# Optimization experiments

Measured on AMD Instinct MI355X. Metric: run time of the kernel, lower is better.

Reference implementation:

```python
import jax, jax.numpy as jnp
import numpy as np

WS = 7          # window size
DIM = 192
HEADS = 6
NW = 64         # number of windows per image (mask leading dim)
NC = 3          # n_contrast (q and kv)
B_ = 1024       # num_windows * batch


def _relative_position_index(ws):
    coords = np.stack(np.meshgrid(np.arange(ws), np.arange(ws), indexing='ij'))  # (2, ws, ws)
    cf = coords.reshape(2, -1)                       # (2, ws*ws)
    rel = cf[:, :, None] - cf[:, None, :]            # (2, N, N)
    rel = rel.transpose(1, 2, 0).copy()              # (N, N, 2)
    rel[:, :, 0] += ws - 1
    rel[:, :, 1] += ws - 1
    rel[:, :, 0] *= 2 * ws - 1
    return rel.sum(-1)                               # (N, N) int

REL_IDX = jnp.asarray(_relative_position_index(WS))


def setup_inputs() -> dict:
    key = jax.random.key(0)
    ks = jax.random.split(key, 13)
    f32 = jnp.float32
    inp = {
        'x_q': jax.random.normal(ks[0], (B_, NC, WS, WS, DIM), f32),
        'x_k': jax.random.normal(ks[1], (B_, NC, WS, WS, DIM), f32),
        'x_v': jax.random.normal(ks[2], (B_, NC, WS, WS, DIM), f32),
        'mask': jax.random.normal(ks[3], (NW, WS * WS, WS * WS), f32),
        # Linear weights stored torch-style: (out_features, in_features)
        'q_w': jax.random.normal(ks[4], (DIM, DIM), f32) * 0.02,
        'q_b': jnp.zeros((DIM,), f32),
        'k_w': jax.random.normal(ks[5], (DIM, DIM), f32) * 0.02,
        'k_b': jnp.zeros((DIM,), f32),
        'v_w': jax.random.normal(ks[6], (DIM, DIM), f32) * 0.02,
        'v_b': jnp.zeros((DIM,), f32),
        'proj_w': jax.random.normal(ks[7], (DIM, DIM), f32) * 0.02,
        'proj_b': jnp.zeros((DIM,), f32),
        'bias_table': jax.random.normal(ks[8], ((2 * WS - 1) ** 2, HEADS), f32) * 0.02,
    }
    return inp


def reference(x_q, x_k, x_v, mask, q_w, q_b, k_w, k_b, v_w, v_b, proj_w, proj_b, bias_table):
    Bw, ncq, Wh, Ww, C = x_q.shape
    nckv = x_k.shape[1]
    H = HEADS
    hd = C // H
    Nq = ncq * Wh * Ww
    Nkv = nckv * Wh * Ww

    xq = x_q.reshape(Bw, Nq, C)
    xk = x_k.reshape(Bw, Nkv, C)
    xv = x_v.reshape(Bw, Nkv, C)

    q = (xq @ q_w.T + q_b).reshape(Bw, Nq, H, hd).transpose(0, 2, 1, 3)   # (B_, H, Nq, hd)
    k = (xk @ k_w.T + k_b).reshape(Bw, Nkv, H, hd).transpose(0, 2, 1, 3)
    v = (xv @ v_w.T + v_b).reshape(Bw, Nkv, H, hd).transpose(0, 2, 1, 3)

    scale = hd ** (-0.5)
    attn = jnp.einsum('bhqd,bhkd->bhqk', q * scale, k)                    # (B_, H, Nq, Nkv)

    Nwin = Wh * Ww
    bias = bias_table[REL_IDX.reshape(-1)].reshape(Nwin, Nwin, H)
    bias = bias.transpose(2, 0, 1)                                        # (H, Nwin, Nwin)
    bias = jnp.tile(bias, (1, ncq, nckv))                                 # (H, Nq, Nkv)
    attn = attn + bias[None]

    nW = mask.shape[0]
    m = jnp.tile(mask, (1, ncq, nckv))                                    # (nW, Nq, Nkv)
    attn = attn.reshape(Bw // nW, nW, H, Nq, Nkv) + m[None, :, None]
    attn = attn.reshape(Bw, H, Nq, Nkv)
    attn = jax.nn.softmax(attn, axis=-1)

    out = jnp.einsum('bhqk,bhkd->bhqd', attn, v)                          # (B_, H, Nq, hd)
    out = out.transpose(0, 2, 1, 3).reshape(Bw, Nq, C)
    out = out @ proj_w.T + proj_b
    return out.reshape(Bw, ncq, Wh, Ww, C)
```

## Files before the change

kernel.cpp:

```cpp
#include <hip/hip_runtime.h>
#include <stdint.h>

#define ROWS 150528
#define QSCALE 0.17677669529663687f
#define L2E 1.44269504088896f

typedef __attribute__((ext_vector_type(8))) __bf16 bf16x8;
typedef __attribute__((ext_vector_type(4))) __bf16 bf16x4;
typedef __attribute__((ext_vector_type(4))) float f32x4;
typedef __attribute__((ext_vector_type(4))) float f4;

static __device__ __forceinline__ f32x4 mfma_bf16(bf16x8 a, bf16x8 b, f32x4 c) {
  return __builtin_amdgcn_mfma_f32_16x16x32_bf16(a, b, c, 0, 0, 0);
}

static __device__ __forceinline__ uint32_t pack_bf16(float a, float b) {
  uint16_t ux = __builtin_bit_cast(uint16_t, (__bf16)a);
  uint16_t uy = __builtin_bit_cast(uint16_t, (__bf16)b);
  return (uint32_t)ux | ((uint32_t)uy << 16);
}

__global__ void cvt4(const float* s0, const float* s1, const float* s2, const float* s3,
                     __bf16* d0, __bf16* d1, __bf16* d2, __bf16* d3) {
  const int y = blockIdx.y;
  const float* s = y == 0 ? s0 : y == 1 ? s1 : y == 2 ? s2 : s3;
  __bf16* d = y == 0 ? d0 : y == 1 ? d1 : y == 2 ? d2 : d3;
  int i = blockIdx.x * 256 + threadIdx.x;
  f4 v = ((const f4*)s)[i];
  bf16x4 b;
  b[0] = (__bf16)v[0]; b[1] = (__bf16)v[1]; b[2] = (__bf16)v[2]; b[3] = (__bf16)v[3];
  ((bf16x4*)d)[i] = b;
}

__global__ void bmpre(const float* __restrict__ maskp, const float* __restrict__ btab,
                      float* __restrict__ bmall) {
  const int win = blockIdx.x, h = blockIdx.y;
  float* dst = bmall + ((size_t)(win * 6 + h)) * 2800;
  for (int i = threadIdx.x; i < 2796; i += 256) {
    int q = i / 57, ke = i - q * 57;
    int k = ke >= 49 ? ke - 49 : ke;
    if (q > 48) q = 48;
    int qi = q / 7, qj = q - qi * 7, ki = k / 7, kj = k - ki * 7;
    int rel = (qi - ki + 6) * 13 + (qj - kj + 6);
    dst[i] = (maskp[win * 2401 + q * 49 + k] + btab[rel * 6 + h]) * L2E;
  }
}

template<bool IN_F32, bool OUT_F32>
static __device__ __forceinline__
void gemm3t(const void* __restrict__ Xv, const __bf16* __restrict__ Wb,
            const float* __restrict__ bias, void* __restrict__ Ov, float scale,
            __bf16* Xs )
{
  const int tid = threadIdx.x;
  const int wv = tid >> 6, lane = tid & 63, lr = lane & 15, lg = lane >> 4;

  bf16x8 wf[3][6];
  float bcol[3];
  #pragma unroll
  for (int t = 0; t < 3; ++t) {
    const int nt = wv + 4 * t;
    const __bf16* wr = &Wb[(nt * 16 + lr) * 192 + lg * 8];
    #pragma unroll
    for (int kk = 0; kk < 6; ++kk) wf[t][kk] = *(const bf16x8*)&wr[kk * 32];
    bcol[t] = bias[nt * 16 + lr] * scale;
  }

  const size_t ti0 = (size_t)blockIdx.x * 3;

  if (IN_F32) {
    const f4* X4 = (const f4*)Xv + ti0 * 64 * 48;
    #pragma unroll
    for (int p = 0; p < 12; ++p) {
      int i = tid + p * 256;
      int r = i / 48, c = i % 48;
      f4 v = X4[i];
      bf16x4 bb;
      bb[0] = (__bf16)v[0]; bb[1] = (__bf16)v[1]; bb[2] = (__bf16)v[2]; bb[3] = (__bf16)v[3];
      *(bf16x4*)&Xs[r * 200 + c * 4] = bb;
    }
  } else {
    const __bf16* X = (const __bf16*)Xv;
    #pragma unroll
    for (int p = 0; p < 6; ++p) {
      int i = tid + p * 256;
      int r = i / 24, c8 = i % 24;
      int hh = c8 >> 2, sub = c8 & 3;
      *(bf16x8*)&Xs[r * 200 + c8 * 8] =
          *(const bf16x8*)&X[((size_t)hh * ROWS + ti0 * 64 + r) * 32 + sub * 8];
    }
  }
  __syncthreads();

  #pragma unroll
  for (int it = 0; it < 3; ++it) {
    const size_t row0 = (ti0 + it) * 64;

    f4 pf[12];
    bf16x8 pf8[6];
    if (it < 2) {
      if (IN_F32) {
        const f4* X4n = (const f4*)Xv + (row0 + 64) * 48;
        #pragma unroll
        for (int p = 0; p < 12; ++p) pf[p] = X4n[tid + p * 256];
      } else {
        const __bf16* X = (const __bf16*)Xv;
        #pragma unroll
        for (int p = 0; p < 6; ++p) {
          int i = tid + p * 256;
          int r = i / 24, c8 = i % 24;
          int hh = c8 >> 2, sub = c8 & 3;
          pf8[p] = *(const bf16x8*)&X[((size_t)hh * ROWS + row0 + 64 + r) * 32 + sub * 8];
        }
      }
    }

    #pragma unroll
    for (int rg = 0; rg < 4; ++rg) {
      bf16x8 a[6];
      const __bf16* xr = &Xs[(rg * 16 + lr) * 200 + lg * 8];
      #pragma unroll
      for (int kk = 0; kk < 6; ++kk) a[kk] = *(const bf16x8*)&xr[kk * 32];
      const size_t grow = row0 + rg * 16 + lg * 4;
      #pragma unroll
      for (int t = 0; t < 3; ++t) {
        f32x4 acc = {0.f, 0.f, 0.f, 0.f};
        #pragma unroll
        for (int kk = 0; kk < 6; ++kk) acc = mfma_bf16(a[kk], wf[t][kk], acc);
        const int nt = wv + 4 * t;
        if (OUT_F32) {
          const int col = nt * 16 + lr;
          #pragma unroll
          for (int j = 0; j < 4; ++j)
            ((float*)Ov)[(grow + j) * 192 + col] = acc[j] * scale + bcol[t];
        } else {
          const int hh = nt >> 1, c32 = (nt & 1) * 16 + lr;
          #pragma unroll
          for (int j = 0; j < 4; ++j)
            ((__bf16*)Ov)[((size_t)hh * ROWS + grow + j) * 32 + c32] =
                (__bf16)(acc[j] * scale + bcol[t]);
        }
      }
    }

    if (it < 2) {
      __syncthreads();
      if (IN_F32) {
        #pragma unroll
        for (int p = 0; p < 12; ++p) {
          int i = tid + p * 256;
          int r = i / 48, c = i % 48;
          bf16x4 bb;
          bb[0] = (__bf16)pf[p][0]; bb[1] = (__bf16)pf[p][1];
          bb[2] = (__bf16)pf[p][2]; bb[3] = (__bf16)pf[p][3];
          *(bf16x4*)&Xs[r * 200 + c * 4] = bb;
        }
      } else {
        #pragma unroll
        for (int p = 0; p < 6; ++p) {
          int i = tid + p * 256;
          int r = i / 24, c8 = i % 24;
          *(bf16x8*)&Xs[r * 200 + c8 * 8] = pf8[p];
        }
      }
      __syncthreads();
    }
  }
}

__global__ __launch_bounds__(256, 2)
void qkvgemm(const float* __restrict__ xq, const float* __restrict__ xk,
             const float* __restrict__ xv,
             const __bf16* __restrict__ wq, const __bf16* __restrict__ wk,
             const __bf16* __restrict__ wv,
             const float* __restrict__ bq, const float* __restrict__ bk,
             const float* __restrict__ bv,
             __bf16* __restrict__ oq, __bf16* __restrict__ ok,
             __bf16* __restrict__ ov)
{
  __shared__ __align__(16) __bf16 Xs[64 * 200];
  const int y = blockIdx.y;
  const float* x = y == 0 ? xq : y == 1 ? xk : xv;
  const __bf16* w = y == 0 ? wq : y == 1 ? wk : wv;
  const float* bi = y == 0 ? bq : y == 1 ? bk : bv;
  __bf16* o = y == 0 ? oq : y == 1 ? ok : ov;
  const float scale = y == 0 ? (QSCALE * L2E) : 1.f;
  gemm3t<true, false>(x, w, bi, o, scale, Xs);
}

__global__ __launch_bounds__(256, 2)
void projgemm(const __bf16* __restrict__ X, const __bf16* __restrict__ Wb,
              const float* __restrict__ bias, float* __restrict__ Ov)
{
  __shared__ __align__(16) __bf16 Xs[64 * 200];
  gemm3t<false, true>(X, Wb, bias, Ov, 1.f, Xs);
}

__global__ __launch_bounds__(320, 5)
void attn8(const __bf16* __restrict__ Q, const __bf16* __restrict__ K,
           const __bf16* __restrict__ V, __bf16* __restrict__ O,
           const float* __restrict__ bmall)
{
  __shared__ __align__(16) __bf16 Ks[160 * 40];
  __shared__ __align__(16) __bf16 Vt[32 * 168];
  __shared__ __align__(16) float bm2[2796];

  const int b = blockIdx.x, h = blockIdx.y;
  const int tid = threadIdx.x;
  const size_t hb = (size_t)h * ROWS + (size_t)b * 147;
  const int wv = tid >> 6, lane = tid & 63;
  const int lr = lane & 15, lg = lane >> 4;

  bf16x8 qf = *(const bf16x8*)&Q[(hb + wv * 16 + lr) * 32 + lg * 8];

  {
    const f4* bsrc = (const f4*)(bmall + (size_t)((b & 63) * 6 + h) * 2800);
    for (int i = tid; i < 699; i += 320) ((f4*)bm2)[i] = bsrc[i];
  }
  for (int i = tid; i < 588; i += 320) {
    int k = i >> 2, c = i & 3;
    int phys = (k & ~31) | (((k >> 2) & 1) << 4) | (((k >> 3) & 3) << 2) | (k & 3);
    *(bf16x8*)&Ks[phys * 40 + c * 8] = *(const bf16x8*)&K[(hb + k) * 32 + c * 8];
  }
  for (int t = tid; t < 588; t += 320) {
    int key = t >> 2, dblk = t & 3;
    bf16x8 v = *(const bf16x8*)&V[(hb + key) * 32 + dblk * 8];
    #pragma unroll
    for (int e = 0; e < 8; ++e) Vt[(dblk * 8 + e) * 168 + key] = v[e];
  }
  for (int i = tid; i < 32 * 13; i += 320) {
    int d = i / 13, key = 147 + (i - (i / 13) * 13);
    Vt[d * 168 + key] = (__bf16)0.f;
  }
  __syncthreads();

  #pragma unroll
  for (int t = 0; t < 2; ++t) {
    const int mt = wv + 5 * t;

    bf16x8 qn = qf;
    if (t == 0) {
      int qr = (wv + 5) * 16 + lr; if (qr > 146) qr = 146;
      qn = *(const bf16x8*)&Q[(hb + qr) * 32 + lg * 8];
    }

    int r = mt * 16 + lr;
    int q49 = r; if (q49 >= 98) q49 -= 98; if (q49 >= 49) q49 -= 49;
    const float* bmrow = &bm2[q49 * 57];

    f32x4 o0 = {0.f,0.f,0.f,0.f}, o1 = {0.f,0.f,0.f,0.f};
    float sum = 0.f;
    int kb = lg * 8;
    #pragma unroll
    for (int s = 0; s < 5; ++s) {
      const f32x4 z = {0.f,0.f,0.f,0.f};
      f32x4 st0 = mfma_bf16(*(const bf16x8*)&Ks[(s * 32 + lr) * 40 + lg * 8], qf, z);
      f32x4 st1 = mfma_bf16(*(const bf16x8*)&Ks[(s * 32 + 16 + lr) * 40 + lg * 8], qf, z);
      const float* bp = bmrow + kb;
      #pragma unroll
      for (int j = 0; j < 4; ++j) { st0[j] += bp[j]; st1[j] += bp[4 + j]; }
      if (s == 4) {
        #pragma unroll
        for (int j = 0; j < 4; ++j) {
          if (lg * 8 + j >= 19) st0[j] = -1e30f;
          if (lg * 8 + j >= 15) st1[j] = -1e30f;
        }
      }
      #pragma unroll
      for (int j = 0; j < 4; ++j) { st0[j] = exp2f(st0[j]); sum += st0[j]; }
      #pragma unroll
      for (int j = 0; j < 4; ++j) { st1[j] = exp2f(st1[j]); sum += st1[j]; }
      union { bf16x8 v; uint32_t w[4]; } pu;
      pu.w[0] = pack_bf16(st0[0], st0[1]);
      pu.w[1] = pack_bf16(st0[2], st0[3]);
      pu.w[2] = pack_bf16(st1[0], st1[1]);
      pu.w[3] = pack_bf16(st1[2], st1[3]);
      bf16x8 v0 = *(const bf16x8*)&Vt[lr * 168 + s * 32 + lg * 8];
      bf16x8 v1 = *(const bf16x8*)&Vt[(16 + lr) * 168 + s * 32 + lg * 8];
      o0 = mfma_bf16(pu.v, v0, o0);
      o1 = mfma_bf16(pu.v, v1, o1);
      kb += 32; if (kb >= 49) kb -= 49;
    }
    sum += __shfl_xor(sum, 16);
    sum += __shfl_xor(sum, 32);
    const float rinv = 1.f / sum;
    #pragma unroll
    for (int j = 0; j < 4; ++j) {
      const int qa = mt * 16 + lg * 4 + j;
      const float rj = __shfl(rinv, lg * 4 + j);
      if (qa < 147) {
        const size_t base = (hb + qa) * 32;
        O[base + lr]      = (__bf16)(o0[j] * rj);
        O[base + 16 + lr] = (__bf16)(o1[j] * rj);
      }
    }
    qf = qn;
  }
}

extern "C" void kernel_launch(void* const* d_in, const int* in_sizes, int n_in,
                              void* d_out, int out_size, void* d_ws, size_t ws_size,
                              hipStream_t stream) {
  (void)in_sizes; (void)n_in; (void)out_size;
  const float* x_q  = (const float*)d_in[0];
  const float* x_k  = (const float*)d_in[1];
  const float* x_v  = (const float*)d_in[2];
  const float* maskp= (const float*)d_in[3];
  const float* q_w  = (const float*)d_in[4];
  const float* q_b  = (const float*)d_in[5];
  const float* k_w  = (const float*)d_in[6];
  const float* k_b  = (const float*)d_in[7];
  const float* v_w  = (const float*)d_in[8];
  const float* v_b  = (const float*)d_in[9];
  const float* p_w  = (const float*)d_in[10];
  const float* p_b  = (const float*)d_in[11];
  const float* btab = (const float*)d_in[12];

  char* ws = (char*)d_ws;
  float* bmall = (float*)ws;
  const size_t bmsz = (size_t)64 * 6 * 2800 * sizeof(float);
  char* wsp = ws + bmsz;
  const size_t wsz = 36864 * sizeof(__bf16);
  __bf16* wq  = (__bf16*)wsp;
  __bf16* wk  = (__bf16*)(wsp + wsz);
  __bf16* wvp = (__bf16*)(wsp + 2 * wsz);
  __bf16* wp  = (__bf16*)(wsp + 3 * wsz);
  char* bufs = wsp + 4 * wsz;
  const size_t sz = (size_t)ROWS * 192 * sizeof(__bf16);
  __bf16* qb = (__bf16*)bufs;
  __bf16* kb = (__bf16*)(bufs + sz);
  __bf16* vb = (__bf16*)(bufs + 2 * sz);
  const size_t need4 = bmsz + 4 * wsz + 4 * sz;
  __bf16* ob = (ws_size >= need4) ? (__bf16*)(bufs + 3 * sz) : qb;

  cvt4<<<dim3(36, 4), 256, 0, stream>>>(q_w, k_w, v_w, p_w, wq, wk, wvp, wp);
  bmpre<<<dim3(64, 6), 256, 0, stream>>>(maskp, btab, bmall);

  qkvgemm<<<dim3(ROWS / 192, 3), 256, 0, stream>>>(x_q, x_k, x_v, wq, wk, wvp,
                                                   q_b, k_b, v_b, qb, kb, vb);

  attn8<<<dim3(1024, 6), 320, 0, stream>>>(qb, kb, vb, ob, bmall);

  projgemm<<<ROWS / 192, 256, 0, stream>>>(ob, wp, p_b, (float*)d_out);
}
```

Baseline: 264.0 us.

## Fuse QKV projection into per-window attention kernel, keeping K/V in LDS

Replaces the separate QKV GEMM and attention kernels with one kernel per window. It projects K and V into shared memory and Q into registers, then runs all six heads' attention from there. The Q weight rows are permuted and pre-scaled so the projected Q lands directly in MFMA operand layout. This removes the bf16 Q/K/V round-trip through global memory and one launch. In exchange each block uses a lot of LDS (about 140 KB) and 640 threads, which limits occupancy, and every block reloads the weight matrices.

```diff
diff --git a/kernel.cpp b/kernel.cpp
--- a/kernel.cpp
+++ b/kernel.cpp
@@ -4,11 +4,13 @@
 #define ROWS 150528
 #define QSCALE 0.17677669529663687f
 #define L2E 1.44269504088896f
+#define QS (QSCALE * L2E)
 
 typedef __attribute__((ext_vector_type(8))) __bf16 bf16x8;
 typedef __attribute__((ext_vector_type(4))) __bf16 bf16x4;
 typedef __attribute__((ext_vector_type(4))) float f32x4;
 typedef __attribute__((ext_vector_type(4))) float f4;
+typedef __attribute__((ext_vector_type(2))) uint32_t u32x2;
 
 static __device__ __forceinline__ f32x4 mfma_bf16(bf16x8 a, bf16x8 b, f32x4 c) {
   return __builtin_amdgcn_mfma_f32_16x16x32_bf16(a, b, c, 0, 0, 0);
@@ -20,16 +22,36 @@
   return (uint32_t)ux | ((uint32_t)uy << 16);
 }
 
+static __device__ __forceinline__ int sigma(int p) {
+  int ct = p >> 4, m = p & 15;
+  return (ct >> 1) * 32 + ((m >> 2) << 3) + ((ct & 1) << 2) + (m & 3);
+}
+
 __global__ void cvt4(const float* s0, const float* s1, const float* s2, const float* s3,
                      __bf16* d0, __bf16* d1, __bf16* d2, __bf16* d3) {
   const int y = blockIdx.y;
-  const float* s = y == 0 ? s0 : y == 1 ? s1 : y == 2 ? s2 : s3;
-  __bf16* d = y == 0 ? d0 : y == 1 ? d1 : y == 2 ? d2 : d3;
   int i = blockIdx.x * 256 + threadIdx.x;
+  if (y == 0) {
+    int p = i / 48, c = i - p * 48;
+    f4 v = ((const f4*)s0)[sigma(p) * 48 + c];
+    bf16x4 b;
+    #pragma unroll
+    for (int e = 0; e < 4; ++e) b[e] = (__bf16)(v[e] * QS);
+    ((bf16x4*)d0)[i] = b;
+    return;
+  }
+  const float* s = y == 1 ? s1 : y == 2 ? s2 : s3;
+  __bf16* d = y == 1 ? d1 : y == 2 ? d2 : d3;
   f4 v = ((const f4*)s)[i];
   bf16x4 b;
-  b[0] = (__bf16)v[0]; b[1] = (__bf16)v[1]; b[2] = (__bf16)v[2]; b[3] = (__bf16)v[3];
+  #pragma unroll
+  for (int e = 0; e < 4; ++e) b[e] = (__bf16)v[e];
   ((bf16x4*)d)[i] = b;
+}
+
+__global__ void bprep(const float* __restrict__ qb, float* __restrict__ bqp) {
+  int p = threadIdx.x;
+  if (p < 192) bqp[p] = qb[sigma(p)] * QS;
 }
 
 __global__ void bmpre(const float* __restrict__ maskp, const float* __restrict__ btab,
@@ -46,11 +68,170 @@
   }
 }
 
+__global__ __launch_bounds__(640, 3)
+void fqkattn(const float* __restrict__ xq, const float* __restrict__ xk,
+             const float* __restrict__ xv,
+             const __bf16* __restrict__ wqp, const __bf16* __restrict__ wkb,
+             const __bf16* __restrict__ wvb,
+             const float* __restrict__ bqp, const float* __restrict__ bk,
+             const float* __restrict__ bv,
+             __bf16* __restrict__ O, const float* __restrict__ bmall)
+{
+  __shared__ __align__(16) __bf16 Ks[38400];
+  __shared__ __align__(16) __bf16 Vt[32256];
+
+  const int b = blockIdx.x;
+  const int tid = threadIdx.x;
+  const int wvn = tid >> 6;
+  const int lane = tid & 63, lr = lane & 15, lg = lane >> 4;
+  const size_t bw = (size_t)b * 147;
+  const int row = wvn * 16 + lr;
+  const int rowc = row > 146 ? 146 : row;
+  const int phys = (row & ~31) | (((row >> 2) & 1) << 4) | (((row >> 3) & 3) << 2) | (row & 3);
+
+  bf16x8 a[6];
+  auto loadA = [&](const float* base) {
+    f4 p0[12];
+    #pragma unroll
+    for (int kk = 0; kk < 6; ++kk) {
+      p0[2 * kk]     = *(const f4*)(base + kk * 32);
+      p0[2 * kk + 1] = *(const f4*)(base + kk * 32 + 4);
+    }
+    #pragma unroll
+    for (int kk = 0; kk < 6; ++kk)
+      #pragma unroll
+      for (int e = 0; e < 4; ++e) {
+        a[kk][e]     = (__bf16)p0[2 * kk][e];
+        a[kk][4 + e] = (__bf16)p0[2 * kk + 1][e];
+      }
+  };
+
+  loadA(&xk[(bw + rowc) * 192 + lg * 8]);
+  for (int ct = 0; ct < 12; ++ct) {
+    bf16x8 wf[6];
+    const __bf16* wr = &wkb[(ct * 16 + lr) * 192 + lg * 8];
+    #pragma unroll
+    for (int kk = 0; kk < 6; ++kk) wf[kk] = *(const bf16x8*)&wr[kk * 32];
+    f32x4 acc = {0.f, 0.f, 0.f, 0.f};
+    #pragma unroll
+    for (int kk = 0; kk < 6; ++kk) acc = mfma_bf16(wf[kk], a[kk], acc);
+    f4 bb = *(const f4*)&bk[ct * 16 + 4 * lg];
+    u32x2 pw;
+    pw[0] = pack_bf16(acc[0] + bb[0], acc[1] + bb[1]);
+    pw[1] = pack_bf16(acc[2] + bb[2], acc[3] + bb[3]);
+    *(u32x2*)&Ks[(ct >> 1) * 6400 + phys * 40 + (ct & 1) * 16 + 4 * lg] = pw;
+  }
+
+  loadA(&xv[(bw + rowc) * 192 + lg * 8]);
+  for (int ct = 0; ct < 12; ++ct) {
+    bf16x8 wf[6];
+    const __bf16* wr = &wvb[(ct * 16 + lr) * 192 + lg * 8];
+    #pragma unroll
+    for (int kk = 0; kk < 6; ++kk) wf[kk] = *(const bf16x8*)&wr[kk * 32];
+    f32x4 acc = {0.f, 0.f, 0.f, 0.f};
+    #pragma unroll
+    for (int kk = 0; kk < 6; ++kk) acc = mfma_bf16(wf[kk], a[kk], acc);
+    f4 bb = *(const f4*)&bv[ct * 16 + 4 * lg];
+    const int d0 = (ct & 1) * 16 + 4 * lg;
+    __bf16* vb8 = &Vt[(ct >> 1) * 5376 + row];
+    #pragma unroll
+    for (int j = 0; j < 4; ++j) vb8[(d0 + j) * 168] = (__bf16)(acc[j] + bb[j]);
+  }
+
+  loadA(&xq[(bw + rowc) * 192 + lg * 8]);
+  bf16x8 qf6[6];
+  #pragma unroll
+  for (int hh = 0; hh < 6; ++hh) {
+    union { bf16x8 v; uint32_t w[4]; } q;
+    #pragma unroll
+    for (int half = 0; half < 2; ++half) {
+      const int ct = hh * 2 + half;
+      bf16x8 wf[6];
+      const __bf16* wr = &wqp[(ct * 16 + lr) * 192 + lg * 8];
+      #pragma unroll
+      for (int kk = 0; kk < 6; ++kk) wf[kk] = *(const bf16x8*)&wr[kk * 32];
+      f32x4 acc = {0.f, 0.f, 0.f, 0.f};
+      #pragma unroll
+      for (int kk = 0; kk < 6; ++kk) acc = mfma_bf16(wf[kk], a[kk], acc);
+      f4 bb = *(const f4*)&bqp[ct * 16 + 4 * lg];
+      q.w[half * 2]     = pack_bf16(acc[0] + bb[0], acc[1] + bb[1]);
+      q.w[half * 2 + 1] = pack_bf16(acc[2] + bb[2], acc[3] + bb[3]);
+    }
+    qf6[hh] = q.v;
+  }
+  __syncthreads();
+
+  int q49 = row; if (q49 >= 98) q49 -= 98; if (q49 >= 49) q49 -= 49;
+  int off[5];
+  {
+    int kb = lg * 8;
+    #pragma unroll
+    for (int s = 0; s < 5; ++s) { off[s] = q49 * 57 + kb; kb += 32; if (kb >= 49) kb -= 49; }
+  }
+  const float* bmb = bmall + (size_t)((b & 63) * 6) * 2800;
+
+  #pragma unroll
+  for (int h = 0; h < 6; ++h) {
+    const float* bmh = bmb + h * 2800;
+    f4 bb0[5], bb1[5];
+    #pragma unroll
+    for (int s = 0; s < 5; ++s) {
+      bb0[s] = *(const f4*)(bmh + off[s]);
+      bb1[s] = *(const f4*)(bmh + off[s] + 4);
+    }
+    const __bf16* kbase = &Ks[h * 6400];
+    const __bf16* vbase = &Vt[h * 5376];
+    f32x4 o0 = {0.f,0.f,0.f,0.f}, o1 = {0.f,0.f,0.f,0.f};
+    float sum = 0.f;
+    #pragma unroll
+    for (int s = 0; s < 5; ++s) {
+      const f32x4 z = {0.f,0.f,0.f,0.f};
+      f32x4 st0 = mfma_bf16(*(const bf16x8*)&kbase[(s * 32 + lr) * 40 + lg * 8], qf6[h], z);
+      f32x4 st1 = mfma_bf16(*(const bf16x8*)&kbase[(s * 32 + 16 + lr) * 40 + lg * 8], qf6[h], z);
+      #pragma unroll
+      for (int j = 0; j < 4; ++j) { st0[j] += bb0[s][j]; st1[j] += bb1[s][j]; }
+      if (s == 4) {
+        #pragma unroll
+        for (int j = 0; j < 4; ++j) {
+          if (lg * 8 + j >= 19) st0[j] = -1e30f;
+          if (lg * 8 + j >= 15) st1[j] = -1e30f;
+        }
+      }
+      #pragma unroll
+      for (int j = 0; j < 4; ++j) { st0[j] = exp2f(st0[j]); sum += st0[j]; }
+      #pragma unroll
+      for (int j = 0; j < 4; ++j) { st1[j] = exp2f(st1[j]); sum += st1[j]; }
+      union { bf16x8 v; uint32_t w[4]; } pu;
+      pu.w[0] = pack_bf16(st0[0], st0[1]);
+      pu.w[1] = pack_bf16(st0[2], st0[3]);
+      pu.w[2] = pack_bf16(st1[0], st1[1]);
+      pu.w[3] = pack_bf16(st1[2], st1[3]);
+      bf16x8 v0 = *(const bf16x8*)&vbase[lr * 168 + s * 32 + lg * 8];
+      bf16x8 v1 = *(const bf16x8*)&vbase[(16 + lr) * 168 + s * 32 + lg * 8];
+      o0 = mfma_bf16(pu.v, v0, o0);
+      o1 = mfma_bf16(pu.v, v1, o1);
+    }
+    sum += __shfl_xor(sum, 16);
+    sum += __shfl_xor(sum, 32);
+    const float rinv = 1.f / sum;
+    #pragma unroll
+    for (int j = 0; j < 4; ++j) {
+      const int qa = wvn * 16 + lg * 4 + j;
+      const float rj = __shfl(rinv, lg * 4 + j);
+      if (qa < 147) {
+        const size_t base = ((size_t)h * ROWS + bw + qa) * 32;
+        O[base + lr]      = (__bf16)(o0[j] * rj);
+        O[base + 16 + lr] = (__bf16)(o1[j] * rj);
+      }
+    }
+  }
+}
+
 template<bool IN_F32, bool OUT_F32>
 static __device__ __forceinline__
 void gemm3t(const void* __restrict__ Xv, const __bf16* __restrict__ Wb,
             const float* __restrict__ bias, void* __restrict__ Ov, float scale,
-            __bf16* Xs )
+            __bf16* Xs)
 {
   const int tid = threadIdx.x;
   const int wv = tid >> 6, lane = tid & 63, lr = lane & 15, lg = lane >> 4;
@@ -68,18 +249,7 @@
 
   const size_t ti0 = (size_t)blockIdx.x * 3;
 
-  if (IN_F32) {
-    const f4* X4 = (const f4*)Xv + ti0 * 64 * 48;
-    #pragma unroll
-    for (int p = 0; p < 12; ++p) {
-      int i = tid + p * 256;
-      int r = i / 48, c = i % 48;
-      f4 v = X4[i];
-      bf16x4 bb;
-      bb[0] = (__bf16)v[0]; bb[1] = (__bf16)v[1]; bb[2] = (__bf16)v[2]; bb[3] = (__bf16)v[3];
-      *(bf16x4*)&Xs[r * 200 + c * 4] = bb;
-    }
-  } else {
+  {
     const __bf16* X = (const __bf16*)Xv;
     #pragma unroll
     for (int p = 0; p < 6; ++p) {
@@ -96,22 +266,15 @@
   for (int it = 0; it < 3; ++it) {
     const size_t row0 = (ti0 + it) * 64;
 
-    f4 pf[12];
     bf16x8 pf8[6];
     if (it < 2) {
-      if (IN_F32) {
-        const f4* X4n = (const f4*)Xv + (row0 + 64) * 48;
-        #pragma unroll
-        for (int p = 0; p < 12; ++p) pf[p] = X4n[tid + p * 256];
-      } else {
-        const __bf16* X = (const __bf16*)Xv;
-        #pragma unroll
-        for (int p = 0; p < 6; ++p) {
-          int i = tid + p * 256;
-          int r = i / 24, c8 = i % 24;
-          int hh = c8 >> 2, sub = c8 & 3;
-          pf8[p] = *(const bf16x8*)&X[((size_t)hh * ROWS + row0 + 64 + r) * 32 + sub * 8];
-        }
+      const __bf16* X = (const __bf16*)Xv;
+      #pragma unroll
+      for (int p = 0; p < 6; ++p) {
+        int i = tid + p * 256;
+        int r = i / 24, c8 = i % 24;
+        int hh = c8 >> 2, sub = c8 & 3;
+        pf8[p] = *(const bf16x8*)&X[((size_t)hh * ROWS + row0 + 64 + r) * 32 + sub * 8];
       }
     }
 
@@ -128,64 +291,24 @@
         #pragma unroll
         for (int kk = 0; kk < 6; ++kk) acc = mfma_bf16(a[kk], wf[t][kk], acc);
         const int nt = wv + 4 * t;
-        if (OUT_F32) {
-          const int col = nt * 16 + lr;
-          #pragma unroll
-          for (int j = 0; j < 4; ++j)
-            ((float*)Ov)[(grow + j) * 192 + col] = acc[j] * scale + bcol[t];
-        } else {
-          const int hh = nt >> 1, c32 = (nt & 1) * 16 + lr;
-          #pragma unroll
-          for (int j = 0; j < 4; ++j)
-            ((__bf16*)Ov)[((size_t)hh * ROWS + grow + j) * 32 + c32] =
-                (__bf16)(acc[j] * scale + bcol[t]);
-        }
+        const int col = nt * 16 + lr;
+        #pragma unroll
+        for (int j = 0; j < 4; ++j)
+          ((float*)Ov)[(grow + j) * 192 + col] = acc[j] * scale + bcol[t];
       }
     }
 
     if (it < 2) {
       __syncthreads();
-      if (IN_F32) {
-        #pragma unroll
-        for (int p = 0; p < 12; ++p) {
-          int i = tid + p * 256;
-          int r = i / 48, c = i % 48;
-          bf16x4 bb;
-          bb[0] = (__bf16)pf[p][0]; bb[1] = (__bf16)pf[p][1];
-          bb[2] = (__bf16)pf[p][2]; bb[3] = (__bf16)pf[p][3];
-          *(bf16x4*)&Xs[r * 200 + c * 4] = bb;
-        }
-      } else {
-        #pragma unroll
-        for (int p = 0; p < 6; ++p) {
-          int i = tid + p * 256;
-          int r = i / 24, c8 = i % 24;
-          *(bf16x8*)&Xs[r * 200 + c8 * 8] = pf8[p];
-        }
+      #pragma unroll
+      for (int p = 0; p < 6; ++p) {
+        int i = tid + p * 256;
+        int r = i / 24, c8 = i % 24;
+        *(bf16x8*)&Xs[r * 200 + c8 * 8] = pf8[p];
       }
       __syncthreads();
     }
   }
-}
-
-__global__ __launch_bounds__(256, 2)
-void qkvgemm(const float* __restrict__ xq, const float* __restrict__ xk,
-             const float* __restrict__ xv,
-             const __bf16* __restrict__ wq, const __bf16* __restrict__ wk,
-             const __bf16* __restrict__ wv,
-             const float* __restrict__ bq, const float* __restrict__ bk,
-             const float* __restrict__ bv,
-             __bf16* __restrict__ oq, __bf16* __restrict__ ok,
-             __bf16* __restrict__ ov)
-{
-  __shared__ __align__(16) __bf16 Xs[64 * 200];
-  const int y = blockIdx.y;
-  const float* x = y == 0 ? xq : y == 1 ? xk : xv;
-  const __bf16* w = y == 0 ? wq : y == 1 ? wk : wv;
-  const float* bi = y == 0 ? bq : y == 1 ? bk : bv;
-  __bf16* o = y == 0 ? oq : y == 1 ? ok : ov;
-  const float scale = y == 0 ? (QSCALE * L2E) : 1.f;
-  gemm3t<true, false>(x, w, bi, o, scale, Xs);
 }
 
 __global__ __launch_bounds__(256, 2)
@@ -196,112 +319,10 @@
   gemm3t<false, true>(X, Wb, bias, Ov, 1.f, Xs);
 }
 
-__global__ __launch_bounds__(320, 5)
-void attn8(const __bf16* __restrict__ Q, const __bf16* __restrict__ K,
-           const __bf16* __restrict__ V, __bf16* __restrict__ O,
-           const float* __restrict__ bmall)
-{
-  __shared__ __align__(16) __bf16 Ks[160 * 40];
-  __shared__ __align__(16) __bf16 Vt[32 * 168];
-  __shared__ __align__(16) float bm2[2796];
-
-  const int b = blockIdx.x, h = blockIdx.y;
-  const int tid = threadIdx.x;
-  const size_t hb = (size_t)h * ROWS + (size_t)b * 147;
-  const int wv = tid >> 6, lane = tid & 63;
-  const int lr = lane & 15, lg = lane >> 4;
-
-  bf16x8 qf = *(const bf16x8*)&Q[(hb + wv * 16 + lr) * 32 + lg * 8];
-
-  {
-    const f4* bsrc = (const f4*)(bmall + (size_t)((b & 63) * 6 + h) * 2800);
-    for (int i = tid; i < 699; i += 320) ((f4*)bm2)[i] = bsrc[i];
-  }
-  for (int i = tid; i < 588; i += 320) {
-    int k = i >> 2, c = i & 3;
-    int phys = (k & ~31) | (((k >> 2) & 1) << 4) | (((k >> 3) & 3) << 2) | (k & 3);
-    *(bf16x8*)&Ks[phys * 40 + c * 8] = *(const bf16x8*)&K[(hb + k) * 32 + c * 8];
-  }
-  for (int t = tid; t < 588; t += 320) {
-    int key = t >> 2, dblk = t & 3;
-    bf16x8 v = *(const bf16x8*)&V[(hb + key) * 32 + dblk * 8];
-    #pragma unroll
-    for (int e = 0; e < 8; ++e) Vt[(dblk * 8 + e) * 168 + key] = v[e];
-  }
-  for (int i = tid; i < 32 * 13; i += 320) {
-    int d = i / 13, key = 147 + (i - (i / 13) * 13);
-    Vt[d * 168 + key] = (__bf16)0.f;
-  }
-  __syncthreads();
-
-  #pragma unroll
-  for (int t = 0; t < 2; ++t) {
-    const int mt = wv + 5 * t;
-
-    bf16x8 qn = qf;
-    if (t == 0) {
-      int qr = (wv + 5) * 16 + lr; if (qr > 146) qr = 146;
-      qn = *(const bf16x8*)&Q[(hb + qr) * 32 + lg * 8];
-    }
-
-    int r = mt * 16 + lr;
-    int q49 = r; if (q49 >= 98) q49 -= 98; if (q49 >= 49) q49 -= 49;
-    const float* bmrow = &bm2[q49 * 57];
-
-    f32x4 o0 = {0.f,0.f,0.f,0.f}, o1 = {0.f,0.f,0.f,0.f};
-    float sum = 0.f;
-    int kb = lg * 8;
-    #pragma unroll
-    for (int s = 0; s < 5; ++s) {
-      const f32x4 z = {0.f,0.f,0.f,0.f};
-      f32x4 st0 = mfma_bf16(*(const bf16x8*)&Ks[(s * 32 + lr) * 40 + lg * 8], qf, z);
-      f32x4 st1 = mfma_bf16(*(const bf16x8*)&Ks[(s * 32 + 16 + lr) * 40 + lg * 8], qf, z);
-      const float* bp = bmrow + kb;
-      #pragma unroll
-      for (int j = 0; j < 4; ++j) { st0[j] += bp[j]; st1[j] += bp[4 + j]; }
-      if (s == 4) {
-        #pragma unroll
-        for (int j = 0; j < 4; ++j) {
-          if (lg * 8 + j >= 19) st0[j] = -1e30f;
-          if (lg * 8 + j >= 15) st1[j] = -1e30f;
-        }
-      }
-      #pragma unroll
-      for (int j = 0; j < 4; ++j) { st0[j] = exp2f(st0[j]); sum += st0[j]; }
-      #pragma unroll
-      for (int j = 0; j < 4; ++j) { st1[j] = exp2f(st1[j]); sum += st1[j]; }
-      union { bf16x8 v; uint32_t w[4]; } pu;
-      pu.w[0] = pack_bf16(st0[0], st0[1]);
-      pu.w[1] = pack_bf16(st0[2], st0[3]);
-      pu.w[2] = pack_bf16(st1[0], st1[1]);
-      pu.w[3] = pack_bf16(st1[2], st1[3]);
-      bf16x8 v0 = *(const bf16x8*)&Vt[lr * 168 + s * 32 + lg * 8];
-      bf16x8 v1 = *(const bf16x8*)&Vt[(16 + lr) * 168 + s * 32 + lg * 8];
-      o0 = mfma_bf16(pu.v, v0, o0);
-      o1 = mfma_bf16(pu.v, v1, o1);
-      kb += 32; if (kb >= 49) kb -= 49;
-    }
-    sum += __shfl_xor(sum, 16);
-    sum += __shfl_xor(sum, 32);
-    const float rinv = 1.f / sum;
-    #pragma unroll
-    for (int j = 0; j < 4; ++j) {
-      const int qa = mt * 16 + lg * 4 + j;
-      const float rj = __shfl(rinv, lg * 4 + j);
-      if (qa < 147) {
-        const size_t base = (hb + qa) * 32;
-        O[base + lr]      = (__bf16)(o0[j] * rj);
-        O[base + 16 + lr] = (__bf16)(o1[j] * rj);
-      }
-    }
-    qf = qn;
-  }
-}
-
 extern "C" void kernel_launch(void* const* d_in, const int* in_sizes, int n_in,
                               void* d_out, int out_size, void* d_ws, size_t ws_size,
                               hipStream_t stream) {
-  (void)in_sizes; (void)n_in; (void)out_size;
+  (void)in_sizes; (void)n_in; (void)out_size; (void)ws_size;
   const float* x_q  = (const float*)d_in[0];
   const float* x_k  = (const float*)d_in[1];
   const float* x_v  = (const float*)d_in[2];
@@ -321,25 +342,19 @@
   const size_t bmsz = (size_t)64 * 6 * 2800 * sizeof(float);
   char* wsp = ws + bmsz;
   const size_t wsz = 36864 * sizeof(__bf16);
-  __bf16* wq  = (__bf16*)wsp;
-  __bf16* wk  = (__bf16*)(wsp + wsz);
-  __bf16* wvp = (__bf16*)(wsp + 2 * wsz);
-  __bf16* wp  = (__bf16*)(wsp + 3 * wsz);
-  char* bufs = wsp + 4 * wsz;
-  const size_t sz = (size_t)ROWS * 192 * sizeof(__bf16);
-  __bf16* qb = (__bf16*)bufs;
-  __bf16* kb = (__bf16*)(bufs + sz);
-  __bf16* vb = (__bf16*)(bufs + 2 * sz);
-  const size_t need4 = bmsz + 4 * wsz + 4 * sz;
-  __bf16* ob = (ws_size >= need4) ? (__bf16*)(bufs + 3 * sz) : qb;
-
-  cvt4<<<dim3(36, 4), 256, 0, stream>>>(q_w, k_w, v_w, p_w, wq, wk, wvp, wp);
+  __bf16* wqp = (__bf16*)wsp;
+  __bf16* wkb = (__bf16*)(wsp + wsz);
+  __bf16* wvb = (__bf16*)(wsp + 2 * wsz);
+  __bf16* wpb = (__bf16*)(wsp + 3 * wsz);
+  float* bqp  = (float*)(wsp + 4 * wsz);
+  __bf16* ob  = (__bf16*)(wsp + 4 * wsz + 1024);
+
+  cvt4<<<dim3(36, 4), 256, 0, stream>>>(q_w, k_w, v_w, p_w, wqp, wkb, wvb, wpb);
+  bprep<<<1, 192, 0, stream>>>(q_b, bqp);
   bmpre<<<dim3(64, 6), 256, 0, stream>>>(maskp, btab, bmall);
 
-  qkvgemm<<<dim3(ROWS / 192, 3), 256, 0, stream>>>(x_q, x_k, x_v, wq, wk, wvp,
-                                                   q_b, k_b, v_b, qb, kb, vb);
-
-  attn8<<<dim3(1024, 6), 320, 0, stream>>>(qb, kb, vb, ob, bmall);
-
-  projgemm<<<ROWS / 192, 256, 0, stream>>>(ob, wp, p_b, (float*)d_out);
-}
+  fqkattn<<<1024, 640, 0, stream>>>(x_q, x_k, x_v, wqp, wkb, wvb,
+                                    bqp, k_b, v_b, ob, bmall);
+
+  projgemm<<<ROWS / 192, 256, 0, stream>>>(ob, wpb, p_b, (float*)d_out);
+}
```

New measurement: 425.8 us. +61.3%, slower.

## Double-buffer GEMM LDS tiles, double rows per block, merge prep kernels

Applied to the files above, without the earlier changes.

Merges the weight-conversion and bias/mask precompute kernels into one launch to save a launch. The QKV and projection GEMMs now process six 64-row tiles per block instead of three, with a double-buffered shared-memory tile that drops one barrier per iteration. Each block now uses twice the LDS and launch bounds drop to one block per SM-equivalent, so occupancy falls and the grid halves, which may reduce latency hiding and load balance.

```diff
diff --git a/kernel.cpp b/kernel.cpp
--- a/kernel.cpp
+++ b/kernel.cpp
@@ -20,35 +20,40 @@
   return (uint32_t)ux | ((uint32_t)uy << 16);
 }
 
-__global__ void cvt4(const float* s0, const float* s1, const float* s2, const float* s3,
-                     __bf16* d0, __bf16* d1, __bf16* d2, __bf16* d3) {
-  const int y = blockIdx.y;
-  const float* s = y == 0 ? s0 : y == 1 ? s1 : y == 2 ? s2 : s3;
-  __bf16* d = y == 0 ? d0 : y == 1 ? d1 : y == 2 ? d2 : d3;
-  int i = blockIdx.x * 256 + threadIdx.x;
-  f4 v = ((const f4*)s)[i];
-  bf16x4 b;
-  b[0] = (__bf16)v[0]; b[1] = (__bf16)v[1]; b[2] = (__bf16)v[2]; b[3] = (__bf16)v[3];
-  ((bf16x4*)d)[i] = b;
-}
-
-__global__ void bmpre(const float* __restrict__ maskp, const float* __restrict__ btab,
-                      float* __restrict__ bmall) {
-  const int win = blockIdx.x, h = blockIdx.y;
-  float* dst = bmall + ((size_t)(win * 6 + h)) * 2800;
-  for (int i = threadIdx.x; i < 2796; i += 256) {
-    int q = i / 57, ke = i - q * 57;
-    int k = ke >= 49 ? ke - 49 : ke;
-    if (q > 48) q = 48;
-    int qi = q / 7, qj = q - qi * 7, ki = k / 7, kj = k - ki * 7;
-    int rel = (qi - ki + 6) * 13 + (qj - kj + 6);
-    dst[i] = (maskp[win * 2401 + q * 49 + k] + btab[rel * 6 + h]) * L2E;
+__global__ void prep(const float* __restrict__ q_w, const float* __restrict__ k_w,
+                     const float* __restrict__ v_w, const float* __restrict__ p_w,
+                     __bf16* __restrict__ wq, __bf16* __restrict__ wk,
+                     __bf16* __restrict__ wv, __bf16* __restrict__ wp,
+                     const float* __restrict__ maskp, const float* __restrict__ btab,
+                     float* __restrict__ bmall) {
+  const int bid = blockIdx.x;
+  if (bid < 144) {
+    const int y = bid / 36;
+    const float* s = y == 0 ? q_w : y == 1 ? k_w : y == 2 ? v_w : p_w;
+    __bf16* d = y == 0 ? wq : y == 1 ? wk : y == 2 ? wv : wp;
+    int i = (bid % 36) * 256 + threadIdx.x;
+    f4 v = ((const f4*)s)[i];
+    bf16x4 b;
+    b[0] = (__bf16)v[0]; b[1] = (__bf16)v[1]; b[2] = (__bf16)v[2]; b[3] = (__bf16)v[3];
+    ((bf16x4*)d)[i] = b;
+  } else {
+    const int idx = bid - 144;
+    const int win = idx / 6, h = idx - win * 6;
+    float* dst = bmall + ((size_t)idx) * 2800;
+    for (int i = threadIdx.x; i < 2796; i += 256) {
+      int q = i / 57, ke = i - q * 57;
+      int k = ke >= 49 ? ke - 49 : ke;
+      if (q > 48) q = 48;
+      int qi = q / 7, qj = q - qi * 7, ki = k / 7, kj = k - ki * 7;
+      int rel = (qi - ki + 6) * 13 + (qj - kj + 6);
+      dst[i] = (maskp[win * 2401 + q * 49 + k] + btab[rel * 6 + h]) * L2E;
+    }
   }
 }
 
 template<bool IN_F32, bool OUT_F32>
 static __device__ __forceinline__
-void gemm3t(const void* __restrict__ Xv, const __bf16* __restrict__ Wb,
+void gemm6t(const void* __restrict__ Xv, const __bf16* __restrict__ Wb,
             const float* __restrict__ bias, void* __restrict__ Ov, float scale,
             __bf16* Xs )
 {
@@ -66,7 +71,7 @@
     bcol[t] = bias[nt * 16 + lr] * scale;
   }
 
-  const size_t ti0 = (size_t)blockIdx.x * 3;
+  const size_t ti0 = (size_t)blockIdx.x * 6;
 
   if (IN_F32) {
     const f4* X4 = (const f4*)Xv + ti0 * 64 * 48;
@@ -93,12 +98,13 @@
   __syncthreads();
 
   #pragma unroll
-  for (int it = 0; it < 3; ++it) {
+  for (int it = 0; it < 6; ++it) {
+    __bf16* rb = &Xs[(it & 1) * 12800];
     const size_t row0 = (ti0 + it) * 64;
 
     f4 pf[12];
     bf16x8 pf8[6];
-    if (it < 2) {
+    if (it < 5) {
       if (IN_F32) {
         const f4* X4n = (const f4*)Xv + (row0 + 64) * 48;
         #pragma unroll
@@ -118,7 +124,7 @@
     #pragma unroll
     for (int rg = 0; rg < 4; ++rg) {
       bf16x8 a[6];
-      const __bf16* xr = &Xs[(rg * 16 + lr) * 200 + lg * 8];
+      const __bf16* xr = &rb[(rg * 16 + lr) * 200 + lg * 8];
       #pragma unroll
       for (int kk = 0; kk < 6; ++kk) a[kk] = *(const bf16x8*)&xr[kk * 32];
       const size_t grow = row0 + rg * 16 + lg * 4;
@@ -143,8 +149,8 @@
       }
     }
 
-    if (it < 2) {
-      __syncthreads();
+    if (it < 5) {
+      __bf16* wb = &Xs[((it + 1) & 1) * 12800];
       if (IN_F32) {
         #pragma unroll
         for (int p = 0; p < 12; ++p) {
@@ -153,14 +159,14 @@
           bf16x4 bb;
           bb[0] = (__bf16)pf[p][0]; bb[1] = (__bf16)pf[p][1];
           bb[2] = (__bf16)pf[p][2]; bb[3] = (__bf16)pf[p][3];
-          *(bf16x4*)&Xs[r * 200 + c * 4] = bb;
+          *(bf16x4*)&wb[r * 200 + c * 4] = bb;
         }
       } else {
         #pragma unroll
         for (int p = 0; p < 6; ++p) {
           int i = tid + p * 256;
           int r = i / 24, c8 = i % 24;
-          *(bf16x8*)&Xs[r * 200 + c8 * 8] = pf8[p];
+          *(bf16x8*)&wb[r * 200 + c8 * 8] = pf8[p];
         }
       }
       __syncthreads();
@@ -168,7 +174,7 @@
   }
 }
 
-__global__ __launch_bounds__(256, 2)
+__global__ __launch_bounds__(256, 1)
 void qkvgemm(const float* __restrict__ xq, const float* __restrict__ xk,
              const float* __restrict__ xv,
              const __bf16* __restrict__ wq, const __bf16* __restrict__ wk,
@@ -178,22 +184,22 @@
              __bf16* __restrict__ oq, __bf16* __restrict__ ok,
              __bf16* __restrict__ ov)
 {
-  __shared__ __align__(16) __bf16 Xs[64 * 200];
+  __shared__ __align__(16) __bf16 Xs[2 * 12800];
   const int y = blockIdx.y;
   const float* x = y == 0 ? xq : y == 1 ? xk : xv;
   const __bf16* w = y == 0 ? wq : y == 1 ? wk : wv;
   const float* bi = y == 0 ? bq : y == 1 ? bk : bv;
   __bf16* o = y == 0 ? oq : y == 1 ? ok : ov;
   const float scale = y == 0 ? (QSCALE * L2E) : 1.f;
-  gemm3t<true, false>(x, w, bi, o, scale, Xs);
-}
-
-__global__ __launch_bounds__(256, 2)
+  gemm6t<true, false>(x, w, bi, o, scale, Xs);
+}
+
+__global__ __launch_bounds__(256, 1)
 void projgemm(const __bf16* __restrict__ X, const __bf16* __restrict__ Wb,
               const float* __restrict__ bias, float* __restrict__ Ov)
 {
-  __shared__ __align__(16) __bf16 Xs[64 * 200];
-  gemm3t<false, true>(X, Wb, bias, Ov, 1.f, Xs);
+  __shared__ __align__(16) __bf16 Xs[2 * 12800];
+  gemm6t<false, true>(X, Wb, bias, Ov, 1.f, Xs);
 }
 
 __global__ __launch_bounds__(320, 5)
@@ -333,13 +339,13 @@
   const size_t need4 = bmsz + 4 * wsz + 4 * sz;
   __bf16* ob = (ws_size >= need4) ? (__bf16*)(bufs + 3 * sz) : qb;
 
-  cvt4<<<dim3(36, 4), 256, 0, stream>>>(q_w, k_w, v_w, p_w, wq, wk, wvp, wp);
-  bmpre<<<dim3(64, 6), 256, 0, stream>>>(maskp, btab, bmall);
-
-  qkvgemm<<<dim3(ROWS / 192, 3), 256, 0, stream>>>(x_q, x_k, x_v, wq, wk, wvp,
+  prep<<<528, 256, 0, stream>>>(q_w, k_w, v_w, p_w, wq, wk, wvp, wp,
+                                maskp, btab, bmall);
+
+  qkvgemm<<<dim3(ROWS / 384, 3), 256, 0, stream>>>(x_q, x_k, x_v, wq, wk, wvp,
                                                    q_b, k_b, v_b, qb, kb, vb);
 
   attn8<<<dim3(1024, 6), 320, 0, stream>>>(qb, kb, vb, ob, bmall);
 
-  projgemm<<<ROWS / 192, 256, 0, stream>>>(ob, wp, p_b, (float*)d_out);
-}
+  projgemm<<<ROWS / 384, 256, 0, stream>>>(ob, wp, p_b, (float*)d_out);
+}
```

Measured after the change: 259.1 us. No clear change (-1.9%).
